# Optimization experiments

Hardware: AMD Instinct MI355X
Metric: run time of the kernel (lower is better)

The kernel has to match this reference:

```python
import jax, jax.numpy as jnp
import numpy as np

# Module constants from __init__ (not learned Parameters in the original).
ALPHA = 1.0
BETA = 1.0
EPSILON = 1e-07
PT_CHANNEL = 4  # emb[:, 4, :] is (log-able) transverse momentum


def setup_inputs() -> dict:
    key = jax.random.key(0)
    # emb: [batch, n_features, n_nodes], strictly positive so log(emb[:,4,:]) is finite
    emb = jax.random.uniform(key, (8, 64, 2048), dtype=jnp.float32, minval=0.05, maxval=1.0)
    return {"emb": emb}


def _sqdist(emb):
    # emb: [b, f, n] -> pairwise squared euclidean distance over feature axis: [b, n, n]
    norms = jnp.sum(emb * emb, axis=1)                      # [b, n]
    gram = jnp.einsum("bfi,bfj->bij", emb, emb)             # [b, n, n]
    return norms[:, :, None] + norms[:, None, :] - 2.0 * gram


def reference(emb):
    sqdist = _sqdist(emb)                                    # [b, n, n]
    pow_momenta = jnp.exp(2.0 * ALPHA * jnp.log(emb[:, PT_CHANNEL, :]))   # [b, n]
    min_momenta = jnp.minimum(pow_momenta[:, :, None], pow_momenta[:, None, :])  # sym_min: [b, n, n]
    d_ij_alpha = sqdist * min_momenta                        # [b, n, n]
    d_min = jnp.min(pow_momenta, axis=1) + EPSILON           # [b]
    d_min = d_min[:, None, None]                             # broadcast as expand_as
    d_ij_center = (d_ij_alpha - d_min) / d_min
    w_ij = jnp.exp(-BETA * d_ij_center)
    return w_ij
```

## Files before the change

### kernel.cpp

```cpp
#include <hip/hip_runtime.h>

#define BB 8
#define FF 64
#define NN 2048
#define EPS 1e-7f
#define PTCH 4
#define BT 128
#define NT (NN / BT)
#define NTRI (NT * (NT + 1) / 2)

typedef float f32x4 __attribute__((ext_vector_type(4)));

__global__ __launch_bounds__(256, 2) void wij_kernel(
    const float* __restrict__ emb, float* __restrict__ out) {
  __shared__ float As[FF][BT];
  __shared__ float Bs[FF][BT];
  __shared__ float sm[4];

  int t = blockIdx.x, it = 0;
  while (t >= NT - it) { t -= NT - it; ++it; }
  const int jt = it + t;
  const int b = blockIdx.y;
  const int i0 = it * BT;
  const int j0 = jt * BT;
  const int tid = threadIdx.x;
  const int tx = tid & 15;
  const int ty = tid >> 4;

  const float* embB = emb + (size_t)b * FF * NN;

  const float* row4 = embB + (size_t)PTCH * NN;
  float x0 = row4[tid], x1 = row4[tid + 256], x2 = row4[tid + 512],
        x3 = row4[tid + 768], x4 = row4[tid + 1024], x5 = row4[tid + 1280],
        x6 = row4[tid + 1536], x7 = row4[tid + 1792];

#pragma unroll
  for (int r = 0; r < 8; ++r) {
    const int idx = tid + 256 * r;
    const int f = idx >> 5;
    const int col = (idx & 31) * 4;
    *(f32x4*)&As[f][col] = *(const f32x4*)&embB[(size_t)f * NN + i0 + col];
    *(f32x4*)&Bs[f][col] = *(const f32x4*)&embB[(size_t)f * NN + j0 + col];
  }

  float pmin = fminf(fminf(fminf(x0 * x0, x1 * x1), fminf(x2 * x2, x3 * x3)),
                     fminf(fminf(x4 * x4, x5 * x5), fminf(x6 * x6, x7 * x7)));
#pragma unroll
  for (int off = 32; off > 0; off >>= 1)
    pmin = fminf(pmin, __shfl_down(pmin, off, 64));
  if ((tid & 63) == 0) sm[tid >> 6] = pmin;

  __syncthreads();

  const float dm = fminf(fminf(sm[0], sm[1]), fminf(sm[2], sm[3])) + EPS;
  const float inv = 1.0f / dm;

  const f32x4 vzero = {0.f, 0.f, 0.f, 0.f};
  f32x4 acc[2][2][4];
#pragma unroll
  for (int ri = 0; ri < 2; ++ri)
#pragma unroll
    for (int rj = 0; rj < 2; ++rj)
#pragma unroll
      for (int m = 0; m < 4; ++m) acc[ri][rj][m] = vzero;
  f32x4 niv[2] = {vzero, vzero};
  f32x4 njv[2] = {vzero, vzero};

#pragma unroll 4
  for (int f = 0; f < FF; ++f) {
    const f32x4 a0 = *(const f32x4*)&As[f][ty * 4];
    const f32x4 a1 = *(const f32x4*)&As[f][64 + ty * 4];
    const f32x4 b0 = *(const f32x4*)&Bs[f][tx * 4];
    const f32x4 b1 = *(const f32x4*)&Bs[f][64 + tx * 4];
    niv[0] += a0 * a0;
    niv[1] += a1 * a1;
    njv[0] += b0 * b0;
    njv[1] += b1 * b1;
#pragma unroll
    for (int m = 0; m < 4; ++m) {
      acc[0][0][m] += a0[m] * b0;
      acc[0][1][m] += a0[m] * b1;
      acc[1][0][m] += a1[m] * b0;
      acc[1][1][m] += a1[m] * b1;
    }
  }

  const f32x4 a40 = *(const f32x4*)&As[PTCH][ty * 4];
  const f32x4 a41 = *(const f32x4*)&As[PTCH][64 + ty * 4];
  const f32x4 b40 = *(const f32x4*)&Bs[PTCH][tx * 4];
  const f32x4 b41 = *(const f32x4*)&Bs[PTCH][64 + tx * 4];
  const f32x4 piv[2] = {a40 * a40, a41 * a41};
  const f32x4 pjv[2] = {b40 * b40, b41 * b41};

#pragma unroll
  for (int ri = 0; ri < 2; ++ri)
#pragma unroll
    for (int rj = 0; rj < 2; ++rj)
#pragma unroll
      for (int m = 0; m < 4; ++m) {
        const f32x4 v = acc[ri][rj][m];
        f32x4 w;
#pragma unroll
        for (int n = 0; n < 4; ++n) {
          float sq = fmaf(-2.0f, v[n], niv[ri][m] + njv[rj][n]);
          float mm = fminf(piv[ri][m], pjv[rj][n]);
          w[n] = __expf(fmaf(sq * mm, -inv, 1.0f));
        }
        acc[ri][rj][m] = w;
      }

  float* outB = out + (size_t)b * NN * NN;

#pragma unroll
  for (int ri = 0; ri < 2; ++ri)
#pragma unroll
    for (int m = 0; m < 4; ++m) {
      const size_t row = (size_t)(i0 + ri * 64 + ty * 4 + m) * NN;
#pragma unroll
      for (int rj = 0; rj < 2; ++rj)
        __builtin_nontemporal_store(acc[ri][rj][m],
                                    (f32x4*)&outB[row + j0 + rj * 64 + tx * 4]);
    }

  if (it != jt) {
#pragma unroll
    for (int rj = 0; rj < 2; ++rj)
#pragma unroll
      for (int n = 0; n < 4; ++n) {
        const size_t row = (size_t)(j0 + rj * 64 + tx * 4 + n) * NN;
#pragma unroll
        for (int ri = 0; ri < 2; ++ri) {
          f32x4 v = {acc[ri][rj][0][n], acc[ri][rj][1][n], acc[ri][rj][2][n],
                     acc[ri][rj][3][n]};
          __builtin_nontemporal_store(
              v, (f32x4*)&outB[row + i0 + ri * 64 + ty * 4]);
        }
      }
  }
}

extern "C" void kernel_launch(void* const* d_in, const int* in_sizes, int n_in,
                              void* d_out, int out_size, void* d_ws,
                              size_t ws_size, hipStream_t stream) {
  const float* emb = (const float*)d_in[0];
  float* out = (float*)d_out;
  (void)d_ws; (void)ws_size; (void)in_sizes; (void)n_in; (void)out_size;

  wij_kernel<<<dim3(NTRI, BB), 256, 0, stream>>>(emb, out);
}
```

Before: 161.5 us.

## Split feature loop into two halves to halve LDS and raise occupancy

Shared-memory tiles shrink from 64 to 32 features per operand, so the feature dimension is loaded and accumulated in two passes separated by barriers. Launch bounds go from 2 to 4 blocks per CU. The squared pt values are saved into a small LDS buffer before the tiles are overwritten. The aim is more resident waves to hide the store-bound epilogue, at the cost of an extra barrier round-trip and serialized loads with no overlap, plus register pressure under the tighter launch bound.

```diff
diff --git a/kernel.cpp b/kernel.cpp
--- a/kernel.cpp
+++ b/kernel.cpp
@@ -2,6 +2,7 @@
 
 #define BB 8
 #define FF 64
+#define FH 32
 #define NN 2048
 #define EPS 1e-7f
 #define PTCH 4
@@ -11,10 +12,11 @@
 
 typedef float f32x4 __attribute__((ext_vector_type(4)));
 
-__global__ __launch_bounds__(256, 2) void wij_kernel(
+__global__ __launch_bounds__(256, 4) void wij_kernel(
     const float* __restrict__ emb, float* __restrict__ out) {
-  __shared__ float As[FF][BT];
-  __shared__ float Bs[FF][BT];
+  __shared__ float As[FH][BT];
+  __shared__ float Bs[FH][BT];
+  __shared__ float pmbuf[2 * BT];
   __shared__ float sm[4];
 
   int t = blockIdx.x, it = 0;
@@ -35,12 +37,13 @@
         x6 = row4[tid + 1536], x7 = row4[tid + 1792];
 
 #pragma unroll
-  for (int r = 0; r < 8; ++r) {
+  for (int r = 0; r < 4; ++r) {
     const int idx = tid + 256 * r;
-    const int f = idx >> 5;
+    const int fl = idx >> 5;
     const int col = (idx & 31) * 4;
-    *(f32x4*)&As[f][col] = *(const f32x4*)&embB[(size_t)f * NN + i0 + col];
-    *(f32x4*)&Bs[f][col] = *(const f32x4*)&embB[(size_t)f * NN + j0 + col];
+    const size_t gofs = (size_t)fl * NN;
+    *(f32x4*)&As[fl][col] = *(const f32x4*)&embB[gofs + i0 + col];
+    *(f32x4*)&Bs[fl][col] = *(const f32x4*)&embB[gofs + j0 + col];
   }
 
   float pmin = fminf(fminf(fminf(x0 * x0, x1 * x1), fminf(x2 * x2, x3 * x3)),
@@ -55,6 +58,9 @@
   const float dm = fminf(fminf(sm[0], sm[1]), fminf(sm[2], sm[3])) + EPS;
   const float inv = 1.0f / dm;
 
+  pmbuf[tid] = (tid < BT) ? As[PTCH][tid] * As[PTCH][tid]
+                          : Bs[PTCH][tid - BT] * Bs[PTCH][tid - BT];
+
   const f32x4 vzero = {0.f, 0.f, 0.f, 0.f};
   f32x4 acc[2][2][4];
 #pragma unroll
@@ -67,11 +73,11 @@
   f32x4 njv[2] = {vzero, vzero};
 
 #pragma unroll 4
-  for (int f = 0; f < FF; ++f) {
-    const f32x4 a0 = *(const f32x4*)&As[f][ty * 4];
-    const f32x4 a1 = *(const f32x4*)&As[f][64 + ty * 4];
-    const f32x4 b0 = *(const f32x4*)&Bs[f][tx * 4];
-    const f32x4 b1 = *(const f32x4*)&Bs[f][64 + tx * 4];
+  for (int fl = 0; fl < FH; ++fl) {
+    const f32x4 a0 = *(const f32x4*)&As[fl][ty * 4];
+    const f32x4 a1 = *(const f32x4*)&As[fl][64 + ty * 4];
+    const f32x4 b0 = *(const f32x4*)&Bs[fl][tx * 4];
+    const f32x4 b1 = *(const f32x4*)&Bs[fl][64 + tx * 4];
     niv[0] += a0 * a0;
     niv[1] += a1 * a1;
     njv[0] += b0 * b0;
@@ -85,12 +91,43 @@
     }
   }
 
-  const f32x4 a40 = *(const f32x4*)&As[PTCH][ty * 4];
-  const f32x4 a41 = *(const f32x4*)&As[PTCH][64 + ty * 4];
-  const f32x4 b40 = *(const f32x4*)&Bs[PTCH][tx * 4];
-  const f32x4 b41 = *(const f32x4*)&Bs[PTCH][64 + tx * 4];
-  const f32x4 piv[2] = {a40 * a40, a41 * a41};
-  const f32x4 pjv[2] = {b40 * b40, b41 * b41};
+  __syncthreads();
+
+#pragma unroll
+  for (int r = 0; r < 4; ++r) {
+    const int idx = tid + 256 * r;
+    const int fl = idx >> 5;
+    const int col = (idx & 31) * 4;
+    const size_t gofs = (size_t)(FH + fl) * NN;
+    *(f32x4*)&As[fl][col] = *(const f32x4*)&embB[gofs + i0 + col];
+    *(f32x4*)&Bs[fl][col] = *(const f32x4*)&embB[gofs + j0 + col];
+  }
+
+  __syncthreads();
+
+#pragma unroll 4
+  for (int fl = 0; fl < FH; ++fl) {
+    const f32x4 a0 = *(const f32x4*)&As[fl][ty * 4];
+    const f32x4 a1 = *(const f32x4*)&As[fl][64 + ty * 4];
+    const f32x4 b0 = *(const f32x4*)&Bs[fl][tx * 4];
+    const f32x4 b1 = *(const f32x4*)&Bs[fl][64 + tx * 4];
+    niv[0] += a0 * a0;
+    niv[1] += a1 * a1;
+    njv[0] += b0 * b0;
+    njv[1] += b1 * b1;
+#pragma unroll
+    for (int m = 0; m < 4; ++m) {
+      acc[0][0][m] += a0[m] * b0;
+      acc[0][1][m] += a0[m] * b1;
+      acc[1][0][m] += a1[m] * b0;
+      acc[1][1][m] += a1[m] * b1;
+    }
+  }
+
+  const f32x4 piv[2] = {*(const f32x4*)&pmbuf[ty * 4],
+                        *(const f32x4*)&pmbuf[64 + ty * 4]};
+  const f32x4 pjv[2] = {*(const f32x4*)&pmbuf[BT + tx * 4],
+                        *(const f32x4*)&pmbuf[BT + 64 + tx * 4]};
 
 #pragma unroll
   for (int ri = 0; ri < 2; ++ri)
```

After: 165.8 us. 2.7% more time.
